# Kernel tuning notes

Hardware: AMD Instinct MI355X
Metric: run time of the kernel (lower is better)

## Reference

```python
import jax, jax.numpy as jnp
import numpy as np

B = 32          # decode batch (one query token per sequence)
HID = 4096      # hidden_size
H = 32          # num_heads
D = 128         # head_dim
BLK = 16        # KV-cache block size (vLLM default)
MAXB = 64       # max blocks per sequence
NBLK = 2048     # total cache blocks
S = MAXB * BLK  # max context length = 1024
ROPE_THETA = 10000.0


def _rope(x, positions):
    # x: [B, H, D], positions: [B] int. GPT-NeoX / Llama half-split rotary.
    half = D // 2
    inv_freq = 1.0 / (ROPE_THETA ** (jnp.arange(0, half, dtype=jnp.float32) / half))
    freqs = positions.astype(jnp.float32)[:, None] * inv_freq[None, :]  # [B, D/2]
    cos = jnp.cos(freqs)[:, None, :]  # [B, 1, D/2]
    sin = jnp.sin(freqs)[:, None, :]
    x1, x2 = x[..., :half], x[..., half:]
    return jnp.concatenate([x1 * cos - x2 * sin, x1 * sin + x2 * cos], axis=-1)


def setup_inputs() -> dict:
    key = jax.random.key(0)
    ks = jax.random.split(key, 8)
    hidden_states = jax.random.normal(ks[0], (B, HID), jnp.float32)
    Wq = jax.random.normal(ks[1], (HID, HID), jnp.float32) * 0.02
    Wk = jax.random.normal(ks[2], (HID, HID), jnp.float32) * 0.02
    Wv = jax.random.normal(ks[3], (HID, HID), jnp.float32) * 0.02
    Wo = jax.random.normal(ks[4], (HID, HID), jnp.float32) * 0.02
    k_cache = jax.random.normal(ks[5], (NBLK, BLK, H, D), jnp.float32)
    v_cache = jax.random.normal(ks[6], (NBLK, BLK, H, D), jnp.float32)
    # each sequence owns MAXB distinct cache blocks (non-contiguous)
    block_tables = jax.random.permutation(ks[7], NBLK)[: B * MAXB].reshape(B, MAXB).astype(jnp.int32)
    context_lens = jax.random.randint(jax.random.fold_in(key, 9), (B,), S // 2, S + 1).astype(jnp.int32)
    positions = context_lens - 1  # current token position
    slot_mapping = (block_tables[jnp.arange(B), positions // BLK] * BLK + positions % BLK).astype(jnp.int32)
    return dict(hidden_states=hidden_states, k_cache=k_cache, v_cache=v_cache,
                Wq=Wq, Wk=Wk, Wv=Wv, Wo=Wo,
                positions=positions, slot_mapping=slot_mapping,
                block_tables=block_tables, context_lens=context_lens)


def reference(hidden_states, k_cache, v_cache, Wq, Wk, Wv, Wo,
              positions, slot_mapping, block_tables, context_lens):
    # QKV projections (bias-free, torch Linear convention: x @ W.T)
    q = (hidden_states @ Wq.T).reshape(B, H, D)
    k = (hidden_states @ Wk.T).reshape(B, H, D)
    v = (hidden_states @ Wv.T).reshape(B, H, D)
    q = _rope(q, positions)
    k = _rope(k, positions)
    # write new k/v into the paged cache at slot_mapping
    kc = k_cache.reshape(NBLK * BLK, H, D).at[slot_mapping].set(k)
    vc = v_cache.reshape(NBLK * BLK, H, D).at[slot_mapping].set(v)
    kc = kc.reshape(NBLK, BLK, H, D)
    vc = vc.reshape(NBLK, BLK, H, D)
    # paged gather: [B, MAXB, BLK, H, D] -> [B, S, H, D]
    keys = kc[block_tables].reshape(B, S, H, D)
    vals = vc[block_tables].reshape(B, S, H, D)
    scores = jnp.einsum('bhd,bshd->bhs', q, keys) * (D ** -0.5)
    valid = jnp.arange(S)[None, :] < context_lens[:, None]  # [B, S]
    scores = jnp.where(valid[:, None, :], scores, jnp.float32(-1e30))
    probs = jax.nn.softmax(scores, axis=-1)
    attn = jnp.einsum('bhs,bshd->bhd', probs, vals).reshape(B, H * D)
    return attn @ Wo.T
```

## Files before the change

kernel.cpp:

```cpp
#include <hip/hip_runtime.h>
#include <math.h>

#define HID 4096
#define B 32
#define H 32
#define D 128
#define KBLK 16
#define MAXB 64
#define CHUNK 256
#define NCHUNK 4

typedef float f4 __attribute__((ext_vector_type(4)));
typedef float f2 __attribute__((ext_vector_type(2)));
#define NT_LD4(p) __builtin_nontemporal_load(reinterpret_cast<const f4*>(p))
#define NT_LD2(p) __builtin_nontemporal_load(reinterpret_cast<const f2*>(p))

template <int MODE>
__global__ __launch_bounds__(256) void gemv_kernel(
    const float* __restrict__ W0, const float* __restrict__ W1, const float* __restrict__ W2,
    const float* __restrict__ x, const int* __restrict__ positions, float* __restrict__ out)
{
    __shared__ float wt[8][256];
    __shared__ float buf[4][8][66];
    const int bid = blockIdx.x;
    const int mat = (MODE == 0) ? (bid >> 9) : 0;
    const int sub = bid & 511;
    const bool rope = (MODE == 0) && (mat < 2);
    const int head = sub >> 4;
    const int p0 = (sub & 15) << 2;
    const float* W = (mat == 0) ? W0 : ((mat == 1) ? W1 : W2);
    float* outp = out + (size_t)mat * (B * HID);

    const int tid = threadIdx.x;
    const int lane = tid & 63;
    const int wid = tid >> 6;
    const int b0 = wid << 3;

    float acc[8][8];
#pragma unroll
    for (int c = 0; c < 8; ++c)
#pragma unroll
        for (int j = 0; j < 8; ++j) acc[c][j] = 0.f;

    for (int k0 = 0; k0 < HID; k0 += 256) {
        __syncthreads();
#pragma unroll
        for (int i = 0; i < 2; ++i) {
            int idx = tid + (i << 8);
            int r = idx >> 6;
            int c4 = idx & 63;
            int cr = rope ? (head * 128 + p0 + (r & 3) + ((r >> 2) << 6))
                          : ((sub << 3) + r);
            f4 v = NT_LD4(&W[(size_t)cr * HID + k0 + (c4 << 2)]);
            *reinterpret_cast<f4*>(&wt[r][c4 << 2]) = v;
        }
        __syncthreads();

        float4 hs4[8];
#pragma unroll
        for (int j = 0; j < 8; ++j)
            hs4[j] = *reinterpret_cast<const float4*>(
                &x[(size_t)(b0 + j) * HID + k0 + (lane << 2)]);

#pragma unroll
        for (int c = 0; c < 8; ++c) {
            float4 w4 = *reinterpret_cast<const float4*>(&wt[c][lane << 2]);
#pragma unroll
            for (int j = 0; j < 8; ++j) {
                acc[c][j] += w4.x * hs4[j].x;
                acc[c][j] += w4.y * hs4[j].y;
                acc[c][j] += w4.z * hs4[j].z;
                acc[c][j] += w4.w * hs4[j].w;
            }
        }
    }

    float res[8];
#pragma unroll
    for (int c = 0; c < 8; ++c) {
#pragma unroll
        for (int j = 0; j < 8; ++j) buf[wid][j][lane] = acc[c][j];
        __builtin_amdgcn_sched_barrier(0);
        const float* rp = &buf[wid][lane >> 3][(lane & 7) << 3];
        float4 a = *reinterpret_cast<const float4*>(rp);
        float4 bb = *reinterpret_cast<const float4*>(rp + 4);
        __builtin_amdgcn_sched_barrier(0);
        float s = ((a.x + a.y) + (a.z + a.w)) + ((bb.x + bb.y) + (bb.z + bb.w));
        s += __shfl_xor(s, 1, 64);
        s += __shfl_xor(s, 2, 64);
        s += __shfl_xor(s, 4, 64);
        res[c] = s;
    }

    const int jme = lane >> 3;
    const int cme = lane & 7;
    float myv;
    if (rope) {
        const float pf = (float)positions[b0 + jme];
        float ro[8];
#pragma unroll
        for (int cc = 0; cc < 4; ++cc) {
            float invf = exp2f(-(float)(p0 + cc) * 0.20762050593046013f);
            float f = pf * invf;
            float cs = cosf(f), sn = sinf(f);
            ro[cc]     = res[cc] * cs - res[cc + 4] * sn;
            ro[cc + 4] = res[cc] * sn + res[cc + 4] * cs;
        }
        myv = ro[0];
#pragma unroll
        for (int cc = 1; cc < 8; ++cc) myv = (cme == cc) ? ro[cc] : myv;
    } else {
        myv = res[0];
#pragma unroll
        for (int cc = 1; cc < 8; ++cc) myv = (cme == cc) ? res[cc] : myv;
    }
    const int colw = rope ? (head * 128 + p0 + (cme & 3) + ((cme >> 2) << 6))
                          : ((sub << 3) + cme);
    outp[(size_t)(b0 + jme) * HID + colw] = myv;
}

__global__ __launch_bounds__(256) void attn_partial_kernel(
    const float* __restrict__ qkv,
    const float* __restrict__ k_cache,
    const float* __restrict__ v_cache,
    const int* __restrict__ block_tables,
    const int* __restrict__ context_lens,
    const int* __restrict__ positions,
    float* __restrict__ pm,
    float* __restrict__ pl,
    float* __restrict__ po)
{
    const int h = blockIdx.x;
    const int c = blockIdx.y;
    const int b = blockIdx.z;
    const int L = context_lens[b];
    const int s0 = c << 8;
    if (s0 >= L) return;
    const int Lc = min(L - s0, CHUNK);
    const int pos = positions[b];
    const int tid = threadIdx.x;

    __shared__ float sc[CHUNK];
    __shared__ float red[8];
    __shared__ int btl[16];
    __shared__ float o4[4][D];

    if (tid < 16) btl[tid] = block_tables[b * MAXB + (c << 4) + tid];
    __syncthreads();

    const float* qptr = qkv + (size_t)b * HID + h * D;
    const float* knew = qkv + (size_t)(B * HID) + (size_t)b * HID + h * D;
    const float* vnew = qkv + (size_t)(2 * B * HID) + (size_t)b * HID + h * D;
    const float scale = 0.088388347648318447f;

    const int hw = tid >> 5;
    const int hl = tid & 31;
    const float4 qv = *reinterpret_cast<const float4*>(qptr + (hl << 2));

    int i = hw;
    for (; i + 24 < Lc; i += 32) {
        const int sA = s0 + i, sB = sA + 8, sC = sA + 16, sD = sA + 24;
        const float* kp0 = (sA == pos) ? knew
            : k_cache + ((size_t)(btl[i >> 4] * KBLK + (sA & 15)) * H + h) * D;
        const float* kp1 = (sB == pos) ? knew
            : k_cache + ((size_t)(btl[(i + 8) >> 4] * KBLK + (sB & 15)) * H + h) * D;
        const float* kp2 = (sC == pos) ? knew
            : k_cache + ((size_t)(btl[(i + 16) >> 4] * KBLK + (sC & 15)) * H + h) * D;
        const float* kp3 = (sD == pos) ? knew
            : k_cache + ((size_t)(btl[(i + 24) >> 4] * KBLK + (sD & 15)) * H + h) * D;
        f4 k0 = NT_LD4(kp0 + (hl << 2));
        f4 k1 = NT_LD4(kp1 + (hl << 2));
        f4 k2 = NT_LD4(kp2 + (hl << 2));
        f4 k3 = NT_LD4(kp3 + (hl << 2));
        float d0 = qv.x * k0[0] + qv.y * k0[1] + qv.z * k0[2] + qv.w * k0[3];
        float d1 = qv.x * k1[0] + qv.y * k1[1] + qv.z * k1[2] + qv.w * k1[3];
        float d2 = qv.x * k2[0] + qv.y * k2[1] + qv.z * k2[2] + qv.w * k2[3];
        float d3 = qv.x * k3[0] + qv.y * k3[1] + qv.z * k3[2] + qv.w * k3[3];
#pragma unroll
        for (int m = 16; m; m >>= 1) {
            d0 += __shfl_xor(d0, m, 64);
            d1 += __shfl_xor(d1, m, 64);
            d2 += __shfl_xor(d2, m, 64);
            d3 += __shfl_xor(d3, m, 64);
        }
        if (hl == 0) {
            sc[i] = d0 * scale; sc[i + 8] = d1 * scale;
            sc[i + 16] = d2 * scale; sc[i + 24] = d3 * scale;
        }
    }
    for (; i < Lc; i += 8) {
        const int sA = s0 + i;
        const float* kp = (sA == pos) ? knew
            : k_cache + ((size_t)(btl[i >> 4] * KBLK + (sA & 15)) * H + h) * D;
        f4 k0 = NT_LD4(kp + (hl << 2));
        float d0 = qv.x * k0[0] + qv.y * k0[1] + qv.z * k0[2] + qv.w * k0[3];
#pragma unroll
        for (int m = 16; m; m >>= 1) d0 += __shfl_xor(d0, m, 64);
        if (hl == 0) sc[i] = d0 * scale;
    }
    for (; i < CHUNK; i += 8)
        if (hl == 0) sc[i] = -1e30f;
    __syncthreads();

    const int w = tid >> 6;
    const float xv = sc[tid];
    float m = xv;
#pragma unroll
    for (int mm = 32; mm; mm >>= 1) m = fmaxf(m, __shfl_xor(m, mm, 64));
    if ((tid & 63) == 0) red[w] = m;
    __syncthreads();
    const float gm = fmaxf(fmaxf(red[0], red[1]), fmaxf(red[2], red[3]));

    float p = (xv > -1e29f) ? __expf(xv - gm) : 0.f;
    sc[tid] = p;
    float l = p;
#pragma unroll
    for (int mm = 32; mm; mm >>= 1) l += __shfl_xor(l, mm, 64);
    if ((tid & 63) == 0) red[4 + w] = l;
    __syncthreads();
    const float gl = red[4] + red[5] + red[6] + red[7];

    const int l2 = (tid & 63) << 1;
    float accx = 0.f, accy = 0.f;
    i = w;
    for (; i + 12 < Lc; i += 16) {
        const int sA = s0 + i, sB = sA + 4, sC = sA + 8, sD = sA + 12;
        const float* vp0 = (sA == pos) ? vnew
            : v_cache + ((size_t)(btl[i >> 4] * KBLK + (sA & 15)) * H + h) * D;
        const float* vp1 = (sB == pos) ? vnew
            : v_cache + ((size_t)(btl[(i + 4) >> 4] * KBLK + (sB & 15)) * H + h) * D;
        const float* vp2 = (sC == pos) ? vnew
            : v_cache + ((size_t)(btl[(i + 8) >> 4] * KBLK + (sC & 15)) * H + h) * D;
        const float* vp3 = (sD == pos) ? vnew
            : v_cache + ((size_t)(btl[(i + 12) >> 4] * KBLK + (sD & 15)) * H + h) * D;
        f2 v0 = NT_LD2(vp0 + l2);
        f2 v1 = NT_LD2(vp1 + l2);
        f2 v2 = NT_LD2(vp2 + l2);
        f2 v3 = NT_LD2(vp3 + l2);
        float p0 = sc[i], p1 = sc[i + 4], p2 = sc[i + 8], p3 = sc[i + 12];
        accx += p0 * v0[0]; accy += p0 * v0[1];
        accx += p1 * v1[0]; accy += p1 * v1[1];
        accx += p2 * v2[0]; accy += p2 * v2[1];
        accx += p3 * v3[0]; accy += p3 * v3[1];
    }
    for (; i < Lc; i += 4) {
        const float* vp = (s0 + i == pos) ? vnew
            : v_cache + ((size_t)(btl[i >> 4] * KBLK + ((s0 + i) & 15)) * H + h) * D;
        f2 v0 = NT_LD2(vp + l2);
        float p0 = sc[i];
        accx += p0 * v0[0]; accy += p0 * v0[1];
    }
    o4[w][l2] = accx;
    o4[w][l2 + 1] = accy;
    __syncthreads();

    const int bh = b * H + h;
    if (tid < D) {
        float o = o4[0][tid] + o4[1][tid] + o4[2][tid] + o4[3][tid];
        po[((size_t)bh * NCHUNK + c) * D + tid] = o;
    } else if (tid == D) {
        pm[bh * NCHUNK + c] = gm;
        pl[bh * NCHUNK + c] = gl;
    }
}

__global__ __launch_bounds__(128) void attn_combine_kernel(
    const float* __restrict__ pm, const float* __restrict__ pl,
    const float* __restrict__ po, const int* __restrict__ context_lens,
    float* __restrict__ attn_out)
{
    const int bh = blockIdx.x;
    const int b = bh >> 5;
    const int tid = threadIdx.x;
    const int nc = (context_lens[b] + CHUNK - 1) >> 8;

    float m = -1e30f;
    for (int c = 0; c < nc; ++c) m = fmaxf(m, pm[bh * NCHUNK + c]);
    float wsum = 0.f, o = 0.f;
    for (int c = 0; c < nc; ++c) {
        float wc = __expf(pm[bh * NCHUNK + c] - m);
        wsum += wc * pl[bh * NCHUNK + c];
        o += wc * po[((size_t)bh * NCHUNK + c) * D + tid];
    }
    attn_out[(size_t)bh * D + tid] = o / wsum;
}

extern "C" void kernel_launch(void* const* d_in, const int* in_sizes, int n_in,
                              void* d_out, int out_size, void* d_ws, size_t ws_size,
                              hipStream_t stream) {
    const float* hs        = (const float*)d_in[0];
    const float* k_cache   = (const float*)d_in[1];
    const float* v_cache   = (const float*)d_in[2];
    const float* Wq        = (const float*)d_in[3];
    const float* Wk        = (const float*)d_in[4];
    const float* Wv        = (const float*)d_in[5];
    const float* Wo        = (const float*)d_in[6];
    const int*   positions = (const int*)d_in[7];
    const int*   block_tables = (const int*)d_in[9];
    const int*   context_lens = (const int*)d_in[10];
    float* out = (float*)d_out;

    float* qkv     = (float*)d_ws;
    float* attn_ws = qkv + (size_t)3 * B * HID;
    float* pm      = attn_ws + (size_t)B * HID;
    float* pl      = pm + (size_t)B * H * NCHUNK;
    float* po      = pl + (size_t)B * H * NCHUNK;

    gemv_kernel<0><<<dim3(3 * 512), 256, 0, stream>>>(Wq, Wk, Wv, hs, positions, qkv);
    attn_partial_kernel<<<dim3(H, NCHUNK, B), 256, 0, stream>>>(
        qkv, k_cache, v_cache, block_tables, context_lens, positions, pm, pl, po);
    attn_combine_kernel<<<dim3(B * H), 128, 0, stream>>>(pm, pl, po, context_lens, attn_ws);
    gemv_kernel<1><<<dim3(512), 256, 0, stream>>>(Wo, Wo, Wo, attn_ws, positions, out);
}
```

Measured before the change: 245.4 us.

## Halve attention chunk size, use 128-thread blocks with float4 V loads

Splits the context into 8 chunks of 128 positions instead of 4 of 256, launching 128-thread blocks, so the split-K attention has twice as many smaller blocks. The PV loop now has each half-warp read full float4 rows of V, the same pattern as the K loop, and reduces across the two half-warps with a shuffle instead of four-way shared-memory partials. The intent is better occupancy and load balance across CUs for the paged gather, plus wider V loads. In exchange, the combine kernel handles more partials and each block carries more fixed overhead.

Result: no change. 246.2 us (+0.3%).

```diff
diff --git a/kernel.cpp b/kernel.cpp
--- a/kernel.cpp
+++ b/kernel.cpp
@@ -7,13 +7,11 @@
 #define D 128
 #define KBLK 16
 #define MAXB 64
-#define CHUNK 256
-#define NCHUNK 4
+#define CHUNK 128
+#define NCHUNK 8
 
 typedef float f4 __attribute__((ext_vector_type(4)));
-typedef float f2 __attribute__((ext_vector_type(2)));
 #define NT_LD4(p) __builtin_nontemporal_load(reinterpret_cast<const f4*>(p))
-#define NT_LD2(p) __builtin_nontemporal_load(reinterpret_cast<const f2*>(p))
 
 template <int MODE>
 __global__ __launch_bounds__(256) void gemv_kernel(
@@ -119,7 +117,7 @@
     outp[(size_t)(b0 + jme) * HID + colw] = myv;
 }
 
-__global__ __launch_bounds__(256) void attn_partial_kernel(
+__global__ __launch_bounds__(128) void attn_partial_kernel(
     const float* __restrict__ qkv,
     const float* __restrict__ k_cache,
     const float* __restrict__ v_cache,
@@ -134,18 +132,18 @@
     const int c = blockIdx.y;
     const int b = blockIdx.z;
     const int L = context_lens[b];
-    const int s0 = c << 8;
+    const int s0 = c << 7;
     if (s0 >= L) return;
     const int Lc = min(L - s0, CHUNK);
     const int pos = positions[b];
     const int tid = threadIdx.x;
 
     __shared__ float sc[CHUNK];
-    __shared__ float red[8];
-    __shared__ int btl[16];
-    __shared__ float o4[4][D];
-
-    if (tid < 16) btl[tid] = block_tables[b * MAXB + (c << 4) + tid];
+    __shared__ float red[4];
+    __shared__ int btl[8];
+    __shared__ float o2[2][D];
+
+    if (tid < 8) btl[tid] = block_tables[b * MAXB + (c << 3) + tid];
     __syncthreads();
 
     const float* qptr = qkv + (size_t)b * HID + h * D;
@@ -158,16 +156,16 @@
     const float4 qv = *reinterpret_cast<const float4*>(qptr + (hl << 2));
 
     int i = hw;
-    for (; i + 24 < Lc; i += 32) {
-        const int sA = s0 + i, sB = sA + 8, sC = sA + 16, sD = sA + 24;
+    for (; i + 12 < Lc; i += 16) {
+        const int sA = s0 + i, sB = sA + 4, sC = sA + 8, sD = sA + 12;
         const float* kp0 = (sA == pos) ? knew
             : k_cache + ((size_t)(btl[i >> 4] * KBLK + (sA & 15)) * H + h) * D;
         const float* kp1 = (sB == pos) ? knew
-            : k_cache + ((size_t)(btl[(i + 8) >> 4] * KBLK + (sB & 15)) * H + h) * D;
+            : k_cache + ((size_t)(btl[(i + 4) >> 4] * KBLK + (sB & 15)) * H + h) * D;
         const float* kp2 = (sC == pos) ? knew
-            : k_cache + ((size_t)(btl[(i + 16) >> 4] * KBLK + (sC & 15)) * H + h) * D;
+            : k_cache + ((size_t)(btl[(i + 8) >> 4] * KBLK + (sC & 15)) * H + h) * D;
         const float* kp3 = (sD == pos) ? knew
-            : k_cache + ((size_t)(btl[(i + 24) >> 4] * KBLK + (sD & 15)) * H + h) * D;
+            : k_cache + ((size_t)(btl[(i + 12) >> 4] * KBLK + (sD & 15)) * H + h) * D;
         f4 k0 = NT_LD4(kp0 + (hl << 2));
         f4 k1 = NT_LD4(kp1 + (hl << 2));
         f4 k2 = NT_LD4(kp2 + (hl << 2));
@@ -184,11 +182,11 @@
             d3 += __shfl_xor(d3, m, 64);
         }
         if (hl == 0) {
-            sc[i] = d0 * scale; sc[i + 8] = d1 * scale;
-            sc[i + 16] = d2 * scale; sc[i + 24] = d3 * scale;
-        }
-    }
-    for (; i < Lc; i += 8) {
+            sc[i] = d0 * scale; sc[i + 4] = d1 * scale;
+            sc[i + 8] = d2 * scale; sc[i + 12] = d3 * scale;
+        }
+    }
+    for (; i < Lc; i += 4) {
         const int sA = s0 + i;
         const float* kp = (sA == pos) ? knew
             : k_cache + ((size_t)(btl[i >> 4] * KBLK + (sA & 15)) * H + h) * D;
@@ -198,7 +196,7 @@
         for (int m = 16; m; m >>= 1) d0 += __shfl_xor(d0, m, 64);
         if (hl == 0) sc[i] = d0 * scale;
     }
-    for (; i < CHUNK; i += 8)
+    for (; i < CHUNK; i += 4)
         if (hl == 0) sc[i] = -1e30f;
     __syncthreads();
 
@@ -209,20 +207,19 @@
     for (int mm = 32; mm; mm >>= 1) m = fmaxf(m, __shfl_xor(m, mm, 64));
     if ((tid & 63) == 0) red[w] = m;
     __syncthreads();
-    const float gm = fmaxf(fmaxf(red[0], red[1]), fmaxf(red[2], red[3]));
+    const float gm = fmaxf(red[0], red[1]);
 
     float p = (xv > -1e29f) ? __expf(xv - gm) : 0.f;
     sc[tid] = p;
     float l = p;
 #pragma unroll
     for (int mm = 32; mm; mm >>= 1) l += __shfl_xor(l, mm, 64);
-    if ((tid & 63) == 0) red[4 + w] = l;
-    __syncthreads();
-    const float gl = red[4] + red[5] + red[6] + red[7];
-
-    const int l2 = (tid & 63) << 1;
-    float accx = 0.f, accy = 0.f;
-    i = w;
+    if ((tid & 63) == 0) red[2 + w] = l;
+    __syncthreads();
+    const float gl = red[2] + red[3];
+
+    f4 oacc = {0.f, 0.f, 0.f, 0.f};
+    i = hw;
     for (; i + 12 < Lc; i += 16) {
         const int sA = s0 + i, sB = sA + 4, sC = sA + 8, sD = sA + 12;
         const float* vp0 = (sA == pos) ? vnew
@@ -233,32 +230,35 @@
             : v_cache + ((size_t)(btl[(i + 8) >> 4] * KBLK + (sC & 15)) * H + h) * D;
         const float* vp3 = (sD == pos) ? vnew
             : v_cache + ((size_t)(btl[(i + 12) >> 4] * KBLK + (sD & 15)) * H + h) * D;
-        f2 v0 = NT_LD2(vp0 + l2);
-        f2 v1 = NT_LD2(vp1 + l2);
-        f2 v2 = NT_LD2(vp2 + l2);
-        f2 v3 = NT_LD2(vp3 + l2);
-        float p0 = sc[i], p1 = sc[i + 4], p2 = sc[i + 8], p3 = sc[i + 12];
-        accx += p0 * v0[0]; accy += p0 * v0[1];
-        accx += p1 * v1[0]; accy += p1 * v1[1];
-        accx += p2 * v2[0]; accy += p2 * v2[1];
-        accx += p3 * v3[0]; accy += p3 * v3[1];
+        f4 v0 = NT_LD4(vp0 + (hl << 2));
+        f4 v1 = NT_LD4(vp1 + (hl << 2));
+        f4 v2 = NT_LD4(vp2 + (hl << 2));
+        f4 v3 = NT_LD4(vp3 + (hl << 2));
+        const float p0 = sc[i], p1 = sc[i + 4], p2 = sc[i + 8], p3 = sc[i + 12];
+        oacc += p0 * v0;
+        oacc += p1 * v1;
+        oacc += p2 * v2;
+        oacc += p3 * v3;
     }
     for (; i < Lc; i += 4) {
         const float* vp = (s0 + i == pos) ? vnew
             : v_cache + ((size_t)(btl[i >> 4] * KBLK + ((s0 + i) & 15)) * H + h) * D;
-        f2 v0 = NT_LD2(vp + l2);
-        float p0 = sc[i];
-        accx += p0 * v0[0]; accy += p0 * v0[1];
-    }
-    o4[w][l2] = accx;
-    o4[w][l2 + 1] = accy;
+        f4 v0 = NT_LD4(vp + (hl << 2));
+        oacc += sc[i] * v0;
+    }
+#pragma unroll
+    for (int k = 0; k < 4; ++k) oacc[k] += __shfl_xor(oacc[k], 32, 64);
+    if (hl < 32 && (tid < 32 || (tid >= 64 && tid < 96))) {
+        *reinterpret_cast<f4*>(&o2[w][hl << 2]) = oacc;
+    }
     __syncthreads();
 
     const int bh = b * H + h;
-    if (tid < D) {
-        float o = o4[0][tid] + o4[1][tid] + o4[2][tid] + o4[3][tid];
+    {
+        float o = o2[0][tid] + o2[1][tid];
         po[((size_t)bh * NCHUNK + c) * D + tid] = o;
-    } else if (tid == D) {
+    }
+    if (tid == 0) {
         pm[bh * NCHUNK + c] = gm;
         pl[bh * NCHUNK + c] = gl;
     }
@@ -272,7 +272,7 @@
     const int bh = blockIdx.x;
     const int b = bh >> 5;
     const int tid = threadIdx.x;
-    const int nc = (context_lens[b] + CHUNK - 1) >> 8;
+    const int nc = (context_lens[b] + CHUNK - 1) >> 7;
 
     float m = -1e30f;
     for (int c = 0; c < nc; ++c) m = fmaxf(m, pm[bh * NCHUNK + c]);
@@ -307,7 +307,7 @@
     float* po      = pl + (size_t)B * H * NCHUNK;
 
     gemv_kernel<0><<<dim3(3 * 512), 256, 0, stream>>>(Wq, Wk, Wv, hs, positions, qkv);
-    attn_partial_kernel<<<dim3(H, NCHUNK, B), 256, 0, stream>>>(
+    attn_partial_kernel<<<dim3(H, NCHUNK, B), 128, 0, stream>>>(
         qkv, k_cache, v_cache, block_tables, context_lens, positions, pm, pl, po);
     attn_combine_kernel<<<dim3(B * H), 128, 0, stream>>>(pm, pl, po, context_lens, attn_ws);
     gemv_kernel<1><<<dim3(512), 256, 0, stream>>>(Wo, Wo, Wo, attn_ws, positions, out);
```

## Restructure GEMV so each wave owns two weight rows, dropping LDS weight staging

Applied to the files above, without the earlier changes.

The GEMV kernel no longer stages an 8x256 weight tile in shared memory behind two barriers per k-step. Each wave now loads its own two weight rows directly from global memory and accumulates against all 32 batch rows, with a larger LDS buffer used only for the final cross-lane reduction. The rope pairing maps onto the two rows per wave (d and d+64). This removes the barriers and the LDS round trip for weights. In exchange each wave reads the activation matrix four times per k-step and holds 64 accumulators, which raises register pressure and activation traffic.

Result: slower. 390.4 us (+59.1%).

```diff
diff --git a/kernel.cpp b/kernel.cpp
--- a/kernel.cpp
+++ b/kernel.cpp
@@ -20,8 +20,7 @@
     const float* __restrict__ W0, const float* __restrict__ W1, const float* __restrict__ W2,
     const float* __restrict__ x, const int* __restrict__ positions, float* __restrict__ out)
 {
-    __shared__ float wt[8][256];
-    __shared__ float buf[4][8][66];
+    __shared__ float buf[4][32][66];
     const int bid = blockIdx.x;
     const int mat = (MODE == 0) ? (bid >> 9) : 0;
     const int sub = bid & 511;
@@ -34,89 +33,87 @@
     const int tid = threadIdx.x;
     const int lane = tid & 63;
     const int wid = tid >> 6;
-    const int b0 = wid << 3;
-
-    float acc[8][8];
-#pragma unroll
-    for (int c = 0; c < 8; ++c)
-#pragma unroll
-        for (int j = 0; j < 8; ++j) acc[c][j] = 0.f;
+
+    const int cr0 = rope ? (head * 128 + p0 + wid)      : ((sub << 3) + wid);
+    const int cr1 = rope ? (head * 128 + p0 + wid + 64) : ((sub << 3) + wid + 4);
+    const float* wp0 = W + (size_t)cr0 * HID;
+    const float* wp1 = W + (size_t)cr1 * HID;
+
+    float acc0[32], acc1[32];
+#pragma unroll
+    for (int j = 0; j < 32; ++j) { acc0[j] = 0.f; acc1[j] = 0.f; }
 
     for (int k0 = 0; k0 < HID; k0 += 256) {
-        __syncthreads();
-#pragma unroll
-        for (int i = 0; i < 2; ++i) {
-            int idx = tid + (i << 8);
-            int r = idx >> 6;
-            int c4 = idx & 63;
-            int cr = rope ? (head * 128 + p0 + (r & 3) + ((r >> 2) << 6))
-                          : ((sub << 3) + r);
-            f4 v = NT_LD4(&W[(size_t)cr * HID + k0 + (c4 << 2)]);
-            *reinterpret_cast<f4*>(&wt[r][c4 << 2]) = v;
-        }
-        __syncthreads();
-
-        float4 hs4[8];
-#pragma unroll
-        for (int j = 0; j < 8; ++j)
-            hs4[j] = *reinterpret_cast<const float4*>(
-                &x[(size_t)(b0 + j) * HID + k0 + (lane << 2)]);
-
-#pragma unroll
-        for (int c = 0; c < 8; ++c) {
-            float4 w4 = *reinterpret_cast<const float4*>(&wt[c][lane << 2]);
+        const int kk = k0 + (lane << 2);
+        f4 w0 = NT_LD4(wp0 + kk);
+        f4 w1 = NT_LD4(wp1 + kk);
+#pragma unroll
+        for (int g = 0; g < 4; ++g) {
+            float4 hs[8];
+#pragma unroll
+            for (int j = 0; j < 8; ++j)
+                hs[j] = *reinterpret_cast<const float4*>(
+                    &x[(size_t)((g << 3) + j) * HID + kk]);
 #pragma unroll
             for (int j = 0; j < 8; ++j) {
-                acc[c][j] += w4.x * hs4[j].x;
-                acc[c][j] += w4.y * hs4[j].y;
-                acc[c][j] += w4.z * hs4[j].z;
-                acc[c][j] += w4.w * hs4[j].w;
+                const int jj = (g << 3) + j;
+                acc0[jj] += w0[0] * hs[j].x + w0[1] * hs[j].y
+                          + w0[2] * hs[j].z + w0[3] * hs[j].w;
+                acc1[jj] += w1[0] * hs[j].x + w1[1] * hs[j].y
+                          + w1[2] * hs[j].z + w1[3] * hs[j].w;
             }
         }
     }
 
-    float res[8];
-#pragma unroll
-    for (int c = 0; c < 8; ++c) {
-#pragma unroll
-        for (int j = 0; j < 8; ++j) buf[wid][j][lane] = acc[c][j];
+    const int bj = lane >> 1;
+    const int hf = lane & 1;
+    float s0, s1;
+    {
+#pragma unroll
+        for (int j = 0; j < 32; ++j) buf[wid][j][lane] = acc0[j];
         __builtin_amdgcn_sched_barrier(0);
-        const float* rp = &buf[wid][lane >> 3][(lane & 7) << 3];
-        float4 a = *reinterpret_cast<const float4*>(rp);
-        float4 bb = *reinterpret_cast<const float4*>(rp + 4);
+        const float* rp = &buf[wid][bj][hf << 5];
+        float t = 0.f;
+#pragma unroll
+        for (int q8 = 0; q8 < 8; ++q8) {
+            float4 a = *reinterpret_cast<const float4*>(rp + (q8 << 2));
+            t += (a.x + a.y) + (a.z + a.w);
+        }
         __builtin_amdgcn_sched_barrier(0);
-        float s = ((a.x + a.y) + (a.z + a.w)) + ((bb.x + bb.y) + (bb.z + bb.w));
-        s += __shfl_xor(s, 1, 64);
-        s += __shfl_xor(s, 2, 64);
-        s += __shfl_xor(s, 4, 64);
-        res[c] = s;
-    }
-
-    const int jme = lane >> 3;
-    const int cme = lane & 7;
+        t += __shfl_xor(t, 1, 64);
+        s0 = t;
+    }
+    {
+#pragma unroll
+        for (int j = 0; j < 32; ++j) buf[wid][j][lane] = acc1[j];
+        __builtin_amdgcn_sched_barrier(0);
+        const float* rp = &buf[wid][bj][hf << 5];
+        float t = 0.f;
+#pragma unroll
+        for (int q8 = 0; q8 < 8; ++q8) {
+            float4 a = *reinterpret_cast<const float4*>(rp + (q8 << 2));
+            t += (a.x + a.y) + (a.z + a.w);
+        }
+        __builtin_amdgcn_sched_barrier(0);
+        t += __shfl_xor(t, 1, 64);
+        s1 = t;
+    }
+
     float myv;
+    int colw;
     if (rope) {
-        const float pf = (float)positions[b0 + jme];
-        float ro[8];
-#pragma unroll
-        for (int cc = 0; cc < 4; ++cc) {
-            float invf = exp2f(-(float)(p0 + cc) * 0.20762050593046013f);
-            float f = pf * invf;
-            float cs = cosf(f), sn = sinf(f);
-            ro[cc]     = res[cc] * cs - res[cc + 4] * sn;
-            ro[cc + 4] = res[cc] * sn + res[cc + 4] * cs;
-        }
-        myv = ro[0];
-#pragma unroll
-        for (int cc = 1; cc < 8; ++cc) myv = (cme == cc) ? ro[cc] : myv;
+        const float pf = (float)positions[bj];
+        const int dd = p0 + wid;
+        const float invf = exp2f(-(float)dd * 0.20762050593046013f);
+        const float f = pf * invf;
+        const float cs = cosf(f), sn = sinf(f);
+        if (hf == 0) { myv = s0 * cs - s1 * sn; colw = cr0; }
+        else         { myv = s0 * sn + s1 * cs; colw = cr1; }
     } else {
-        myv = res[0];
-#pragma unroll
-        for (int cc = 1; cc < 8; ++cc) myv = (cme == cc) ? res[cc] : myv;
-    }
-    const int colw = rope ? (head * 128 + p0 + (cme & 3) + ((cme >> 2) << 6))
-                          : ((sub << 3) + cme);
-    outp[(size_t)(b0 + jme) * HID + colw] = myv;
+        myv = (hf == 0) ? s0 : s1;
+        colw = (hf == 0) ? cr0 : cr1;
+    }
+    outp[(size_t)bj * HID + colw] = myv;
 }
 
 __global__ __launch_bounds__(256) void attn_partial_kernel(
```
